# Kernel tuning notes

Measured on AMD Instinct MI355X. Metric: run time of the kernel, lower is better.

## Reference

```python
import jax, jax.numpy as jnp
import numpy as np

EMBED_DIM = 64
HEAD_NUM = 16
BS, QL, KL = 4, 2048, 2048


def setup_inputs() -> dict:
    key = jax.random.key(0)
    k1, k2, k3, k4, k5, k6, k7, k8 = jax.random.split(key, 8)
    d, H = EMBED_DIM, HEAD_NUM
    q_origin = jax.random.normal(k1, (BS, QL, d), dtype=jnp.float32)
    k_origin = jax.random.normal(k2, (BS, KL, d), dtype=jnp.float32)
    mask = jax.random.randint(k3, (BS, QL, KL), 0, 2).astype(bool)
    scale = 1.0 / np.sqrt(d)
    Wq = jax.random.normal(k4, (d, d * H), dtype=jnp.float32) * scale
    Wk = jax.random.normal(k5, (d, d * H), dtype=jnp.float32) * scale
    Wv = jax.random.normal(k6, (d, d * H), dtype=jnp.float32) * scale
    Wfc = jax.random.normal(k7, (d, d), dtype=jnp.float32) * scale
    bfc = jax.random.normal(k8, (d,), dtype=jnp.float32) * 0.01
    return {"q_origin": q_origin, "k_origin": k_origin, "mask": mask,
            "Wq": Wq, "Wk": Wk, "Wv": Wv, "Wfc": Wfc, "bfc": bfc}


def reference(q_origin, k_origin, mask, Wq, Wk, Wv, Wfc, bfc):
    bs, ql, d = q_origin.shape
    _, kl, _ = k_origin.shape
    H = Wq.shape[1] // d
    # projections, split into H heads of width d
    q = (q_origin @ Wq).reshape(bs, ql, H, d)   # bqhd
    k = (k_origin @ Wk).reshape(bs, kl, H, d)   # bkhd
    v = (k_origin @ Wv).reshape(bs, kl, H, d)   # bkhd
    scores = jnp.einsum('bqhd,bkhd->bhqk', q, k)
    scores = jnp.where(mask[:, None, :, :], -jnp.inf, scores)
    attn = jax.nn.softmax(scores / jnp.sqrt(jnp.asarray(d, scores.dtype)), axis=-1)
    attn = jnp.nan_to_num(attn)
    out = jnp.einsum('bhqk,bkhd->bqhd', attn, v)
    # torch code concatenates heads along the sequence axis: (bs, ql*H, d)
    out = out.reshape(bs, ql * H, d)
    return jnp.tanh(out @ Wfc + bfc)
```

## Files before the change

kernel.cpp:

```cpp
#include <hip/hip_runtime.h>
#include <hip/hip_bf16.h>

#define BSZ 4
#define SEQ 2048
#define NH  16
#define DH  64
#define TOK (BSZ*SEQ)
#define PROJC (NH*DH)

typedef __bf16 bf16x8 __attribute__((ext_vector_type(8)));
typedef float  f32x4  __attribute__((ext_vector_type(4)));
typedef float  f32x16 __attribute__((ext_vector_type(16)));
typedef unsigned int uint4v __attribute__((ext_vector_type(4)));
typedef unsigned int uint2v __attribute__((ext_vector_type(2)));

__device__ inline unsigned short f2bf(float f) {
    __bf16 h = (__bf16)f;
    return __builtin_bit_cast(unsigned short, h);
}

__device__ inline bf16x8 ld8(const unsigned short* p) {
    return __builtin_bit_cast(bf16x8, *reinterpret_cast<const uint4v*>(p));
}

__device__ inline float fexp2(float x) {
    float r;
    asm("v_exp_f32 %0, %1" : "=v"(r) : "v"(x));
    return r;
}

__device__ inline void gload16(const unsigned short* g, unsigned short* l) {
    __builtin_amdgcn_global_load_lds(
        (__attribute__((address_space(1))) void*)g,
        (__attribute__((address_space(3))) void*)l, 16, 0, 0);
}

__global__ __launch_bounds__(256) void prep_kernel(const float* __restrict__ q,
                                                   const float* __restrict__ k,
                                                   const float* __restrict__ Wq,
                                                   const float* __restrict__ Wk,
                                                   const float* __restrict__ Wv,
                                                   const float* __restrict__ Wfc,
                                                   unsigned short* __restrict__ qbf,
                                                   unsigned short* __restrict__ kbf,
                                                   unsigned short* __restrict__ WqT,
                                                   unsigned short* __restrict__ WkT,
                                                   unsigned short* __restrict__ WvT,
                                                   unsigned short* __restrict__ WfcT) {
    int bx = blockIdx.x;
    if (bx < 4096) {
        int idx = (bx & 2047) * 256 + threadIdx.x;
        if (bx < 2048) qbf[idx] = f2bf(q[idx]);
        else           kbf[idx] = f2bf(k[idx]);
        return;
    }
    bx -= 4096;
    const float* W; unsigned short* WT; int cols; int base;
    if      (bx < 256) { W = Wq;  WT = WqT;  cols = PROJC; base = bx; }
    else if (bx < 512) { W = Wk;  WT = WkT;  cols = PROJC; base = bx - 256; }
    else if (bx < 768) { W = Wv;  WT = WvT;  cols = PROJC; base = bx - 512; }
    else               { W = Wfc; WT = WfcT; cols = 64;    base = bx - 768; }
    int idx = base * 256 + threadIdx.x;
    int c = idx % cols, kk = idx / cols;
    WT[c * 64 + kk] = f2bf(W[kk * cols + c]);
}

__global__ __launch_bounds__(256) void maskpack_kernel(const int* __restrict__ mask,
                                                       unsigned long long* __restrict__ mbits) {
    size_t gid = (size_t)blockIdx.x * 256 + threadIdx.x;
    int lane = threadIdx.x & 63;
    unsigned long long bal = __ballot(mask[gid] != 0);
    if (lane == 0) mbits[gid >> 6] = bal;
}

__global__ __launch_bounds__(256) void proj_kernel(const unsigned short* __restrict__ qbf,
                                                   const unsigned short* __restrict__ kbf,
                                                   const unsigned short* __restrict__ WqT,
                                                   const unsigned short* __restrict__ WkT,
                                                   const unsigned short* __restrict__ WvT,
                                                   unsigned short* __restrict__ Qo,
                                                   unsigned short* __restrict__ Ko,
                                                   unsigned short* __restrict__ Vto) {
    __shared__ __align__(16) unsigned short T[64][72];
    int z = blockIdx.z;
    const unsigned short* A  = (z == 0) ? qbf : kbf;
    const unsigned short* WT = (z == 0) ? WqT : (z == 1) ? WkT : WvT;
    int tid = threadIdx.x, w = tid >> 6, lane = tid & 63;
    int l15 = lane & 15, l4 = lane >> 4;
    int r0 = blockIdx.x * 64 + w * 16;
    int c0 = blockIdx.y * 64;
    int b = blockIdx.x >> 5;
    size_t bh = (size_t)(b * NH + blockIdx.y);

    const unsigned short* ap = A + (r0 + l15) * 64 + l4 * 8;
    bf16x8 a0 = ld8(ap), a1 = ld8(ap + 32);

    #pragma unroll
    for (int ct = 0; ct < 4; ++ct) {
        const unsigned short* wp = WT + (c0 + ct * 16 + l15) * 64 + l4 * 8;
        bf16x8 b0 = ld8(wp), b1 = ld8(wp + 32);
        f32x4 acc = {0.f, 0.f, 0.f, 0.f};
        if (z == 2) {
            acc = __builtin_amdgcn_mfma_f32_16x16x32_bf16(a0, b0, acc, 0, 0, 0);
            acc = __builtin_amdgcn_mfma_f32_16x16x32_bf16(a1, b1, acc, 0, 0, 0);
        } else {
            acc = __builtin_amdgcn_mfma_f32_16x16x32_bf16(b0, a0, acc, 0, 0, 0);
            acc = __builtin_amdgcn_mfma_f32_16x16x32_bf16(b1, a1, acc, 0, 0, 0);
        }
        uint2v pk;
        pk.x = (unsigned)f2bf(acc[0]) | ((unsigned)f2bf(acc[1]) << 16);
        pk.y = (unsigned)f2bf(acc[2]) | ((unsigned)f2bf(acc[3]) << 16);
        if (z == 2) {
            *reinterpret_cast<uint2v*>(&T[ct * 16 + l15][w * 16 + l4 * 4]) = pk;
        } else {
            *reinterpret_cast<uint2v*>(&T[w * 16 + l15][ct * 16 + l4 * 4]) = pk;
        }
    }
    __syncthreads();

    int rl8 = tid >> 3, chunk = tid & 7;
    int q0 = (blockIdx.x & 31) * 64;
    if (z == 2) {
        #pragma unroll
        for (int p = 0; p < 2; ++p) {
            int dd = p * 32 + rl8;
            uint4v v = *reinterpret_cast<const uint4v*>(&T[dd][chunk * 8]);
            *reinterpret_cast<uint4v*>(Vto + (bh * 64 + dd) * SEQ + q0 + chunk * 8) = v;
        }
    } else {
        unsigned short* dst = (z == 0) ? Qo : Ko;
        #pragma unroll
        for (int p = 0; p < 2; ++p) {
            int rl = p * 32 + rl8;
            uint4v v = *reinterpret_cast<const uint4v*>(&T[rl][chunk * 8]);
            *reinterpret_cast<uint4v*>(dst + (bh * SEQ + q0 + rl) * 64 + chunk * 8) = v;
        }
    }
}

__global__ __launch_bounds__(256, 4) void attn_kernel(const unsigned short* __restrict__ Q,
                                                      const unsigned short* __restrict__ K,
                                                      const unsigned short* __restrict__ Vt,
                                                      const unsigned long long* __restrict__ mbits,
                                                      unsigned short* __restrict__ O) {
    __shared__ __align__(16) unsigned short Ks[2][64 * 64];
    __shared__ __align__(16) unsigned short Vs[2][64 * 64];
    int tid = threadIdx.x, w = tid >> 6, lane = tid & 63;
    int l31 = lane & 31, hi = lane >> 5;
    int hi4 = hi * 4;

    int bid = blockIdx.x;
    int swz = (bid & 7) * 128 + (bid >> 3);
    int bh = swz >> 4;
    int qt = swz & 15;
    int b = bh >> 4;
    int qbase = qt * 128 + w * 32;

    const unsigned short* Qh = Q  + (size_t)bh * SEQ * 64;
    const unsigned short* Kh = K  + (size_t)bh * SEQ * 64;
    const unsigned short* Vh = Vt + (size_t)bh * 64 * SEQ;
    const unsigned long long* mrow =
        mbits + ((size_t)b * SEQ + qbase + l31) * (SEQ / 64);

    int row1 = (w << 3) + (lane >> 3);
    int row2 = row1 + 32;
    int sc1 = (lane & 7) ^ (row1 & 7);
    unsigned short* Kd0 = &Ks[0][0] + w * 512;
    unsigned short* Vd0 = &Vs[0][0] + w * 512;
    unsigned short* Kd1 = &Ks[1][0] + w * 512;
    unsigned short* Vd1 = &Vs[1][0] + w * 512;

    bf16x8 qf[4];
    #pragma unroll
    for (int s = 0; s < 4; ++s)
        qf[s] = ld8(Qh + (size_t)(qbase + l31) * 64 + s * 16 + hi * 8);

    bf16x8 ones;
    #pragma unroll
    for (int i = 0; i < 8; ++i) ones[i] = (__bf16)1.0f;

    f32x16 o0 = {0.f,0.f,0.f,0.f,0.f,0.f,0.f,0.f,0.f,0.f,0.f,0.f,0.f,0.f,0.f,0.f};
    f32x16 o1 = o0;
    f32x16 ellD = o0;
    const float C = 0.125f * 1.44269504088896f;

    auto stage_tile = [&](unsigned short* Kd, unsigned short* Vd, int nkb) {
        gload16(Kh + (size_t)(nkb + row1) * 64 + sc1 * 8, Kd);
        gload16(Kh + (size_t)(nkb + row2) * 64 + sc1 * 8, Kd + 2048);
        gload16(Vh + (size_t)row1 * SEQ + nkb + sc1 * 8, Vd);
        gload16(Vh + (size_t)row2 * SEQ + nkb + sc1 * 8, Vd + 2048);
    };

    auto compute_tile = [&](const unsigned short* Kc, const unsigned short* Vc, int kb) {
        unsigned long long wb = mrow[kb >> 6];
        #pragma unroll
        for (int kt = 0; kt < 2; ++kt) {
            f32x16 z = {0.f,0.f,0.f,0.f,0.f,0.f,0.f,0.f,0.f,0.f,0.f,0.f,0.f,0.f,0.f,0.f};
            int krow = kt * 32 + l31;
            #pragma unroll
            for (int s = 0; s < 4; ++s) {
                const unsigned short* kp =
                    Kc + krow * 64 + ((((s << 1) + hi) ^ (krow & 7)) << 3);
                z = __builtin_amdgcn_mfma_f32_32x32x16_bf16(ld8(kp), qf[s], z, 0, 0, 0);
            }
            unsigned wsh = (unsigned)(wb >> (kt * 32)) >> hi4;
            unsigned wpk[8];
            #pragma unroll
            for (int rq = 0; rq < 4; ++rq) {
                #pragma unroll
                for (int rr = 0; rr < 2; ++rr) {
                    float e[2];
                    #pragma unroll
                    for (int j = 0; j < 2; ++j) {
                        int pos = rq * 8 + 2 * rr + j;
                        int sx = (int)(wsh << (31 - pos)) >> 31;
                        float bias = __builtin_bit_cast(float, (unsigned)sx & 0xFF800000u);
                        e[j] = fexp2(__builtin_fmaf(z[rq * 4 + 2 * rr + j], C, bias));
                    }
                    wpk[rq * 2 + rr] = (unsigned)f2bf(e[0]) | ((unsigned)f2bf(e[1]) << 16);
                }
            }
            __builtin_amdgcn_s_setprio(1);
            #pragma unroll
            for (int sl = 0; sl < 2; ++sl) {
                uint4v aw = {wpk[sl * 4 + 0], wpk[sl * 4 + 1],
                             wpk[sl * 4 + 2], wpk[sl * 4 + 3]};
                bf16x8 af = __builtin_bit_cast(bf16x8, aw);
                ellD = __builtin_amdgcn_mfma_f32_32x32x16_bf16(af, ones, ellD, 0, 0, 0);
                int n = kt * 2 + sl;
                {
                    int vrow = l31;
                    int c0i = ((2 * n) ^ (vrow & 7)) << 3;
                    int c1i = ((2 * n + 1) ^ (vrow & 7)) << 3;
                    uint2v lo = *reinterpret_cast<const uint2v*>(Vc + vrow * 64 + c0i + hi4);
                    uint2v hh = *reinterpret_cast<const uint2v*>(Vc + vrow * 64 + c1i + hi4);
                    uint4v vw = {lo.x, lo.y, hh.x, hh.y};
                    o0 = __builtin_amdgcn_mfma_f32_32x32x16_bf16(
                        af, __builtin_bit_cast(bf16x8, vw), o0, 0, 0, 0);
                }
                {
                    int vrow = 32 + l31;
                    int c0i = ((2 * n) ^ (vrow & 7)) << 3;
                    int c1i = ((2 * n + 1) ^ (vrow & 7)) << 3;
                    uint2v lo = *reinterpret_cast<const uint2v*>(Vc + vrow * 64 + c0i + hi4);
                    uint2v hh = *reinterpret_cast<const uint2v*>(Vc + vrow * 64 + c1i + hi4);
                    uint4v vw = {lo.x, lo.y, hh.x, hh.y};
                    o1 = __builtin_amdgcn_mfma_f32_32x32x16_bf16(
                        af, __builtin_bit_cast(bf16x8, vw), o1, 0, 0, 0);
                }
            }
            __builtin_amdgcn_s_setprio(0);
        }
    };

    stage_tile(Kd0, Vd0, 0);
    __syncthreads();

    for (int kb = 0; kb < SEQ; kb += 128) {
        stage_tile(Kd1, Vd1, kb + 64);
        compute_tile(&Ks[0][0], &Vs[0][0], kb);
        __syncthreads();
        if (kb + 128 < SEQ) stage_tile(Kd0, Vd0, kb + 128);
        compute_tile(&Ks[1][0], &Vs[1][0], kb + 64);
        __syncthreads();
    }
    #pragma unroll
    for (int reg = 0; reg < 16; ++reg) {
        float l = ellD[reg];
        float rcp = (l == 0.f) ? 0.f : __builtin_amdgcn_rcpf(l);
        int ql = (reg & 3) + 8 * (reg >> 2) + hi4;
        size_t base = ((size_t)bh * SEQ + qbase + ql) * 64 + l31;
        O[base]      = f2bf(o0[reg] * rcp);
        O[base + 32] = f2bf(o1[reg] * rcp);
    }
}

__global__ __launch_bounds__(256) void fc_kernel(const unsigned short* __restrict__ O,
                                                 const unsigned short* __restrict__ WfcT,
                                                 const float* __restrict__ bfc,
                                                 float* __restrict__ out) {
    int tid = threadIdx.x, w = tid >> 6, lane = tid & 63;
    int l15 = lane & 15, l4 = lane >> 4;
    int r0 = blockIdx.x * 64 + w * 16;

    int row = r0 + l15;
    int h = row & 15, t_ = row >> 4;
    int q = t_ & 2047, b = t_ >> 11;
    const unsigned short* op = O + (((size_t)(b * NH + h)) * SEQ + q) * 64 + l4 * 8;
    bf16x8 a0 = ld8(op), a1 = ld8(op + 32);

    for (int ct = 0; ct < 4; ++ct) {
        const unsigned short* wp = WfcT + (ct * 16 + l15) * 64 + l4 * 8;
        bf16x8 b0 = ld8(wp), b1 = ld8(wp + 32);
        f32x4 acc = {0.f, 0.f, 0.f, 0.f};
        acc = __builtin_amdgcn_mfma_f32_16x16x32_bf16(b0, a0, acc, 0, 0, 0);
        acc = __builtin_amdgcn_mfma_f32_16x16x32_bf16(b1, a1, acc, 0, 0, 0);
        f32x4 bv = *reinterpret_cast<const f32x4*>(bfc + ct * 16 + l4 * 4);
        f32x4 st;
        #pragma unroll
        for (int r = 0; r < 4; ++r) {
            float x = acc[r] + bv[r];
            x = fminf(fmaxf(x, -9.f), 9.f);
            float t = fexp2(x * 2.88539008177793f);
            st[r] = (t - 1.f) * __builtin_amdgcn_rcpf(t + 1.f);
        }
        *reinterpret_cast<f32x4*>(out + (size_t)row * 64 + ct * 16 + l4 * 4) = st;
    }
}

extern "C" void kernel_launch(void* const* d_in, const int* in_sizes, int n_in,
                              void* d_out, int out_size, void* d_ws, size_t ws_size,
                              hipStream_t stream) {
    const float* q_origin = (const float*)d_in[0];
    const float* k_origin = (const float*)d_in[1];
    const int*   mask     = (const int*)d_in[2];
    const float* Wq       = (const float*)d_in[3];
    const float* Wk       = (const float*)d_in[4];
    const float* Wv       = (const float*)d_in[5];
    const float* Wfc      = (const float*)d_in[6];
    const float* bfc      = (const float*)d_in[7];
    float* out = (float*)d_out;

    unsigned short* ws = (unsigned short*)d_ws;
    unsigned short* qbf  = ws;
    unsigned short* kbf  = qbf  + TOK * DH;
    unsigned short* WqT  = kbf  + TOK * DH;
    unsigned short* WkT  = WqT  + 64 * PROJC;
    unsigned short* WvT  = WkT  + 64 * PROJC;
    unsigned short* WfcT = WvT  + 64 * PROJC;
    unsigned short* Qb   = WfcT + 64 * 64;
    unsigned short* Kb   = Qb   + (size_t)BSZ * NH * SEQ * DH;
    unsigned short* Vtb  = Kb   + (size_t)BSZ * NH * SEQ * DH;
    unsigned short* Ob   = Vtb  + (size_t)BSZ * NH * SEQ * DH;
    unsigned long long* mbits = (unsigned long long*)d_ws;

    prep_kernel<<<4880, 256, 0, stream>>>(q_origin, k_origin, Wq, Wk, Wv, Wfc,
                                          qbf, kbf, WqT, WkT, WvT, WfcT);
    proj_kernel<<<dim3(TOK / 64, PROJC / 64, 3), 256, 0, stream>>>(
        qbf, kbf, WqT, WkT, WvT, Qb, Kb, Vtb);
    maskpack_kernel<<<(size_t)BSZ * SEQ * SEQ / 256, 256, 0, stream>>>(mask, mbits);
    attn_kernel<<<1024, 256, 0, stream>>>(Qb, Kb, Vtb, mbits, Ob);
    fc_kernel<<<(size_t)BSZ * SEQ * NH / 64, 256, 0, stream>>>(Ob, WfcT, bfc, out);
}
```

Baseline: 183.2 us.

## Fuse Q/K/V projections per block and double attention block to 256 query rows

The projection kernel now computes the Q, K and V outputs in one block instead of three z-slices, so the K input rows are loaded once and shared between K and V. The attention kernel moves to 512 threads covering 256 query rows, so each staged K/V tile is reused by eight waves and each thread issues half as many staging loads. This cuts global traffic for K/V tiles and halves the number of attention blocks (512 instead of 1024). The trade-off is fewer blocks to fill the GPU, and launch_bounds(512,4) may limit registers per thread.

```diff
diff --git a/kernel.cpp b/kernel.cpp
--- a/kernel.cpp
+++ b/kernel.cpp
@@ -81,64 +81,63 @@
                                                    unsigned short* __restrict__ Qo,
                                                    unsigned short* __restrict__ Ko,
                                                    unsigned short* __restrict__ Vto) {
-    __shared__ __align__(16) unsigned short T[64][72];
-    int z = blockIdx.z;
-    const unsigned short* A  = (z == 0) ? qbf : kbf;
-    const unsigned short* WT = (z == 0) ? WqT : (z == 1) ? WkT : WvT;
+    __shared__ __align__(16) unsigned short TQ[64][72];
+    __shared__ __align__(16) unsigned short TK[64][72];
+    __shared__ __align__(16) unsigned short TV[64][72];
     int tid = threadIdx.x, w = tid >> 6, lane = tid & 63;
     int l15 = lane & 15, l4 = lane >> 4;
     int r0 = blockIdx.x * 64 + w * 16;
-    int c0 = blockIdx.y * 64;
+    int h = blockIdx.y;
+    int c0 = h * 64;
     int b = blockIdx.x >> 5;
-    size_t bh = (size_t)(b * NH + blockIdx.y);
-
-    const unsigned short* ap = A + (r0 + l15) * 64 + l4 * 8;
-    bf16x8 a0 = ld8(ap), a1 = ld8(ap + 32);
+    size_t bh = (size_t)(b * NH + h);
+
+    const unsigned short* aq = qbf + (r0 + l15) * 64 + l4 * 8;
+    bf16x8 a0q = ld8(aq), a1q = ld8(aq + 32);
+    const unsigned short* ak = kbf + (r0 + l15) * 64 + l4 * 8;
+    bf16x8 a0k = ld8(ak), a1k = ld8(ak + 32);
 
     #pragma unroll
     for (int ct = 0; ct < 4; ++ct) {
-        const unsigned short* wp = WT + (c0 + ct * 16 + l15) * 64 + l4 * 8;
-        bf16x8 b0 = ld8(wp), b1 = ld8(wp + 32);
-        f32x4 acc = {0.f, 0.f, 0.f, 0.f};
-        if (z == 2) {
-            acc = __builtin_amdgcn_mfma_f32_16x16x32_bf16(a0, b0, acc, 0, 0, 0);
-            acc = __builtin_amdgcn_mfma_f32_16x16x32_bf16(a1, b1, acc, 0, 0, 0);
-        } else {
-            acc = __builtin_amdgcn_mfma_f32_16x16x32_bf16(b0, a0, acc, 0, 0, 0);
-            acc = __builtin_amdgcn_mfma_f32_16x16x32_bf16(b1, a1, acc, 0, 0, 0);
-        }
-        uint2v pk;
-        pk.x = (unsigned)f2bf(acc[0]) | ((unsigned)f2bf(acc[1]) << 16);
-        pk.y = (unsigned)f2bf(acc[2]) | ((unsigned)f2bf(acc[3]) << 16);
-        if (z == 2) {
-            *reinterpret_cast<uint2v*>(&T[ct * 16 + l15][w * 16 + l4 * 4]) = pk;
-        } else {
-            *reinterpret_cast<uint2v*>(&T[w * 16 + l15][ct * 16 + l4 * 4]) = pk;
-        }
+        int wrow = (c0 + ct * 16 + l15) * 64 + l4 * 8;
+        bf16x8 q0 = ld8(WqT + wrow), q1 = ld8(WqT + wrow + 32);
+        bf16x8 k0 = ld8(WkT + wrow), k1 = ld8(WkT + wrow + 32);
+        bf16x8 v0 = ld8(WvT + wrow), v1 = ld8(WvT + wrow + 32);
+        f32x4 accq = {0.f,0.f,0.f,0.f}, acck = accq, accv = accq;
+        accq = __builtin_amdgcn_mfma_f32_16x16x32_bf16(q0, a0q, accq, 0, 0, 0);
+        accq = __builtin_amdgcn_mfma_f32_16x16x32_bf16(q1, a1q, accq, 0, 0, 0);
+        acck = __builtin_amdgcn_mfma_f32_16x16x32_bf16(k0, a0k, acck, 0, 0, 0);
+        acck = __builtin_amdgcn_mfma_f32_16x16x32_bf16(k1, a1k, acck, 0, 0, 0);
+        accv = __builtin_amdgcn_mfma_f32_16x16x32_bf16(a0k, v0, accv, 0, 0, 0);
+        accv = __builtin_amdgcn_mfma_f32_16x16x32_bf16(a1k, v1, accv, 0, 0, 0);
+        uint2v pq, pk, pv;
+        pq.x = (unsigned)f2bf(accq[0]) | ((unsigned)f2bf(accq[1]) << 16);
+        pq.y = (unsigned)f2bf(accq[2]) | ((unsigned)f2bf(accq[3]) << 16);
+        pk.x = (unsigned)f2bf(acck[0]) | ((unsigned)f2bf(acck[1]) << 16);
+        pk.y = (unsigned)f2bf(acck[2]) | ((unsigned)f2bf(acck[3]) << 16);
+        pv.x = (unsigned)f2bf(accv[0]) | ((unsigned)f2bf(accv[1]) << 16);
+        pv.y = (unsigned)f2bf(accv[2]) | ((unsigned)f2bf(accv[3]) << 16);
+        *reinterpret_cast<uint2v*>(&TQ[w * 16 + l15][ct * 16 + l4 * 4]) = pq;
+        *reinterpret_cast<uint2v*>(&TK[w * 16 + l15][ct * 16 + l4 * 4]) = pk;
+        *reinterpret_cast<uint2v*>(&TV[ct * 16 + l15][w * 16 + l4 * 4]) = pv;
     }
     __syncthreads();
 
     int rl8 = tid >> 3, chunk = tid & 7;
     int q0 = (blockIdx.x & 31) * 64;
-    if (z == 2) {
-        #pragma unroll
-        for (int p = 0; p < 2; ++p) {
-            int dd = p * 32 + rl8;
-            uint4v v = *reinterpret_cast<const uint4v*>(&T[dd][chunk * 8]);
-            *reinterpret_cast<uint4v*>(Vto + (bh * 64 + dd) * SEQ + q0 + chunk * 8) = v;
-        }
-    } else {
-        unsigned short* dst = (z == 0) ? Qo : Ko;
-        #pragma unroll
-        for (int p = 0; p < 2; ++p) {
-            int rl = p * 32 + rl8;
-            uint4v v = *reinterpret_cast<const uint4v*>(&T[rl][chunk * 8]);
-            *reinterpret_cast<uint4v*>(dst + (bh * SEQ + q0 + rl) * 64 + chunk * 8) = v;
-        }
-    }
-}
-
-__global__ __launch_bounds__(256, 4) void attn_kernel(const unsigned short* __restrict__ Q,
+    #pragma unroll
+    for (int p = 0; p < 2; ++p) {
+        int rl = p * 32 + rl8;
+        uint4v vq = *reinterpret_cast<const uint4v*>(&TQ[rl][chunk * 8]);
+        uint4v vk = *reinterpret_cast<const uint4v*>(&TK[rl][chunk * 8]);
+        uint4v vv = *reinterpret_cast<const uint4v*>(&TV[rl][chunk * 8]);
+        *reinterpret_cast<uint4v*>(Qo  + (bh * SEQ + q0 + rl) * 64 + chunk * 8) = vq;
+        *reinterpret_cast<uint4v*>(Ko  + (bh * SEQ + q0 + rl) * 64 + chunk * 8) = vk;
+        *reinterpret_cast<uint4v*>(Vto + (bh * 64 + rl) * SEQ + q0 + chunk * 8) = vv;
+    }
+}
+
+__global__ __launch_bounds__(512, 4) void attn_kernel(const unsigned short* __restrict__ Q,
                                                       const unsigned short* __restrict__ K,
                                                       const unsigned short* __restrict__ Vt,
                                                       const unsigned long long* __restrict__ mbits,
@@ -150,11 +149,11 @@
     int hi4 = hi * 4;
 
     int bid = blockIdx.x;
-    int swz = (bid & 7) * 128 + (bid >> 3);
-    int bh = swz >> 4;
-    int qt = swz & 15;
+    int swz = (bid & 7) * 64 + (bid >> 3);
+    int bh = swz >> 3;
+    int qt = swz & 7;
     int b = bh >> 4;
-    int qbase = qt * 128 + w * 32;
+    int qbase = qt * 256 + w * 32;
 
     const unsigned short* Qh = Q  + (size_t)bh * SEQ * 64;
     const unsigned short* Kh = K  + (size_t)bh * SEQ * 64;
@@ -163,7 +162,6 @@
         mbits + ((size_t)b * SEQ + qbase + l31) * (SEQ / 64);
 
     int row1 = (w << 3) + (lane >> 3);
-    int row2 = row1 + 32;
     int sc1 = (lane & 7) ^ (row1 & 7);
     unsigned short* Kd0 = &Ks[0][0] + w * 512;
     unsigned short* Vd0 = &Vs[0][0] + w * 512;
@@ -186,9 +184,7 @@
 
     auto stage_tile = [&](unsigned short* Kd, unsigned short* Vd, int nkb) {
         gload16(Kh + (size_t)(nkb + row1) * 64 + sc1 * 8, Kd);
-        gload16(Kh + (size_t)(nkb + row2) * 64 + sc1 * 8, Kd + 2048);
         gload16(Vh + (size_t)row1 * SEQ + nkb + sc1 * 8, Vd);
-        gload16(Vh + (size_t)row2 * SEQ + nkb + sc1 * 8, Vd + 2048);
     };
 
     auto compute_tile = [&](const unsigned short* Kc, const unsigned short* Vc, int kb) {
@@ -336,9 +332,9 @@
 
     prep_kernel<<<4880, 256, 0, stream>>>(q_origin, k_origin, Wq, Wk, Wv, Wfc,
                                           qbf, kbf, WqT, WkT, WvT, WfcT);
-    proj_kernel<<<dim3(TOK / 64, PROJC / 64, 3), 256, 0, stream>>>(
+    proj_kernel<<<dim3(TOK / 64, NH), 256, 0, stream>>>(
         qbf, kbf, WqT, WkT, WvT, Qb, Kb, Vtb);
     maskpack_kernel<<<(size_t)BSZ * SEQ * SEQ / 256, 256, 0, stream>>>(mask, mbits);
-    attn_kernel<<<1024, 256, 0, stream>>>(Qb, Kb, Vtb, mbits, Ob);
+    attn_kernel<<<512, 512, 0, stream>>>(Qb, Kb, Vtb, mbits, Ob);
     fc_kernel<<<(size_t)BSZ * SEQ * NH / 64, 256, 0, stream>>>(Ob, WfcT, bfc, out);
 }
```

Result: faster. 175.0 us (-4.4%).
